# Performance work log

Hardware: AMD Instinct MI355X
Metric: run time of the kernel (lower is better)

Reference implementation:

```python
import jax, jax.numpy as jnp
import numpy as np

N = 100000
DIM = 128
E = 3200000


def setup_inputs() -> dict:
    key = jax.random.key(0)
    k1, k2, k3, k4 = jax.random.split(key, 4)
    x = jax.random.normal(k1, (N, DIM), dtype=jnp.float32)
    edge_index = jax.random.randint(k2, (2, E), 0, N, dtype=jnp.int64)
    # GCNConv params: glorot-style weight [dim, dim], zero-init bias
    W = jax.random.normal(k3, (DIM, DIM), dtype=jnp.float32) * (1.0 / np.sqrt(DIM))
    b = jnp.zeros((DIM,), dtype=jnp.float32)
    return {"x": x, "edge_index": edge_index, "W": W, "b": b}


def gcn_conv(x, edge_index, W, b):
    n = x.shape[0]
    # add self-loops (PyG default add_self_loops=True)
    loop = jnp.arange(n, dtype=edge_index.dtype)
    row = jnp.concatenate([edge_index[0], loop])  # source
    col = jnp.concatenate([edge_index[1], loop])  # target (aggregation index)
    # symmetric normalization D^-1/2 (A+I) D^-1/2; degree counted on targets
    deg = jax.ops.segment_sum(jnp.ones_like(col, dtype=x.dtype), col, num_segments=n)
    dinv = jnp.where(deg > 0, jax.lax.rsqrt(deg), 0.0)
    norm = dinv[row] * dinv[col]  # [E+N]
    xw = x @ W  # dense transform first (dim small)
    msgs = xw[row] * norm[:, None]  # gather + scale
    out = jax.ops.segment_sum(msgs, col, num_segments=n)  # scatter-add
    return out + b


def reference(x, edge_index, W, b):
    # NOTE: original torch loop recomputes from the same x every iteration,
    # so the result equals a single relu(GCNConv(x, edge_index)).
    return jax.nn.relu(gcn_conv(x, edge_index, W, b))
```

## Files before the change

### kernel.cpp

```cpp
#include <hip/hip_runtime.h>

#define DIM 128
#define E_FIXED 3200000
#define BSH 6
#define BNODES 64
#define NB 1600
#define BCAP 2816
#define NBLK 256
#define CAPS 1600
#define XS 136

typedef __attribute__((ext_vector_type(8))) short bf16x8;
typedef __attribute__((ext_vector_type(4))) float f32x4;

__device__ __forceinline__ float bflo(unsigned int w) { return __uint_as_float(w << 16); }
__device__ __forceinline__ float bfhi(unsigned int w) { return __uint_as_float(w & 0xffff0000u); }
__device__ __forceinline__ unsigned short f2bf(float f) {
    union { float f; unsigned int u; } c; c.f = f;
    unsigned int u = c.u + 0x7FFFu + ((c.u >> 16) & 1u);
    return (unsigned short)(u >> 16);
}

__device__ __forceinline__ int edge_shift(const int* __restrict__ edge, int force64) {
    int w = edge[2 * (threadIdx.x & 63) + 1];
    unsigned long long nz = __ballot(w != 0);
    return force64 ? 1 : (nz ? 0 : 1);
}

__global__ __launch_bounds__(1024) void hist_kernel(const int* __restrict__ edge,
                                                    int force64,
                                                    int* __restrict__ hist_g, int E) {
    __shared__ int h[NB];
    const int sh = edge_shift(edge, force64);
    const int tid = threadIdx.x;
    const int k = blockIdx.x;
    for (int b = tid; b < NB; b += 1024) h[b] = 0;
    __syncthreads();

    const int cpb = (E + NBLK - 1) / NBLK;
    const int e0 = k * cpb;
    const int e1 = min(E, e0 + cpb);
    for (int e = e0 + tid; e < e1; e += 1024) {
        int c = edge[((size_t)(E + e)) << sh];
        atomicAdd(&h[c >> BSH], 1);
    }
    __syncthreads();
    for (int b = tid; b < NB; b += 1024) hist_g[(size_t)k * NB + b] = h[b];
}

__global__ __launch_bounds__(NBLK) void prefix_kernel(const int* __restrict__ hist_g,
                                                      int* __restrict__ pre_t,
                                                      int* __restrict__ total) {
    __shared__ int sc[2][NBLK];
    const int b = blockIdx.x;
    const int t = threadIdx.x;
    int v = hist_g[(size_t)t * NB + b];
    sc[0][t] = v;
    __syncthreads();
    int buf = 0;
#pragma unroll
    for (int off = 1; off < NBLK; off <<= 1) {
        sc[buf ^ 1][t] = sc[buf][t] + ((t >= off) ? sc[buf][t - off] : 0);
        buf ^= 1;
        __syncthreads();
    }
    pre_t[(size_t)b * NBLK + t] = sc[buf][t] - v;
    if (t == NBLK - 1) total[b] = sc[buf][t];
}

__global__ __launch_bounds__(512) void scatter_kernel(const int* __restrict__ edge,
                                                      int force64,
                                                      const int* __restrict__ pre_t,
                                                      int* __restrict__ bucketed, int E) {
    __shared__ int cur[NB];
    const int sh = edge_shift(edge, force64);
    const int tid = threadIdx.x;
    const int k = blockIdx.x;
    for (int b = tid; b < NB; b += 512) cur[b] = pre_t[(size_t)b * NBLK + k];
    __syncthreads();

    const int cpb = (E + NBLK - 1) / NBLK;
    const int e0 = k * cpb;
    const int e1 = min(E, e0 + cpb);
    for (int e = e0 + tid; e < e1; e += 512) {
        int r = edge[((size_t)e) << sh];
        int c = edge[((size_t)(E + e)) << sh];
        int b = c >> BSH;
        int pos = atomicAdd(&cur[b], 1);
        if (pos < BCAP)
            bucketed[(size_t)b * BCAP + pos] = (r << BSH) | (c & (BNODES - 1));
    }
}

__global__ __launch_bounds__(256) void degree_kernel(const int* __restrict__ bucketed,
                                                     const int* __restrict__ total,
                                                     int* __restrict__ deg, int n) {
    __shared__ int h[BNODES];
    const int b = blockIdx.x, t = threadIdx.x;
    if (t < BNODES) h[t] = 0;
    __syncthreads();
    const int m = min(total[b], BCAP);
    const int* seg = bucketed + (size_t)b * BCAP;
    for (int i = t; i < m; i += 256) atomicAdd(&h[seg[i] & (BNODES - 1)], 1);
    __syncthreads();
    int gnode = (b << BSH) + t;
    if (t < BNODES && gnode < n) deg[gnode] = h[t];
}

__global__ __launch_bounds__(256) void gemm_kernel(const float* __restrict__ x,
                                                   const float* __restrict__ W,
                                                   const int* __restrict__ deg,
                                                   unsigned short* __restrict__ xws, int n) {
    __shared__ unsigned short xb[64 * XS];
    __shared__ unsigned short wt[128 * XS];
    __shared__ float sdn[64];
    const int tid = threadIdx.x;
    const int base = blockIdx.x * 64;

#pragma unroll
    for (int it = 0; it < 8; ++it) {
        int idx = it * 256 + tid;
        int r = idx >> 5;
        int k4 = idx & 31;
        int gr = base + r;
        float4 v = make_float4(0.f, 0.f, 0.f, 0.f);
        if (gr < n) v = ((const float4*)(x + (size_t)gr * DIM))[k4];
        ushort4 u;
        u.x = f2bf(v.x); u.y = f2bf(v.y); u.z = f2bf(v.z); u.w = f2bf(v.w);
        *(ushort4*)&xb[r * XS + k4 * 4] = u;
    }
#pragma unroll
    for (int it = 0; it < 16; ++it) {
        int idx = it * 256 + tid;
        int k = idx >> 5;
        int c4 = idx & 31;
        float4 v = ((const float4*)(W + (size_t)k * DIM))[c4];
        wt[(c4 * 4 + 0) * XS + k] = f2bf(v.x);
        wt[(c4 * 4 + 1) * XS + k] = f2bf(v.y);
        wt[(c4 * 4 + 2) * XS + k] = f2bf(v.z);
        wt[(c4 * 4 + 3) * XS + k] = f2bf(v.w);
    }
    if (tid < 64) {
        int gn = base + tid;
        int d = (gn < n) ? deg[gn] : 0;
        sdn[tid] = rsqrtf((float)(d + 1));
    }
    __syncthreads();

    const int w = tid >> 6, lane = tid & 63;
    const int lrow = lane & 15, kgrp = lane >> 4;
    const unsigned short* arow = &xb[(w * 16 + lrow) * XS + kgrp * 8];
    const unsigned short* bbase = &wt[lrow * XS + kgrp * 8];

    const int lr0 = w * 16 + kgrp * 4;
    const float dv0 = sdn[lr0 + 0], dv1 = sdn[lr0 + 1];
    const float dv2 = sdn[lr0 + 2], dv3 = sdn[lr0 + 3];
    const int grow0 = base + lr0;

    bf16x8 a0 = *(const bf16x8*)(arow + 0);
    bf16x8 a1 = *(const bf16x8*)(arow + 32);
    bf16x8 a2 = *(const bf16x8*)(arow + 64);
    bf16x8 a3 = *(const bf16x8*)(arow + 96);

#pragma unroll
    for (int ct = 0; ct < 8; ++ct) {
        const unsigned short* bcol = bbase + ct * 16 * XS;
        f32x4 acc = {0.f, 0.f, 0.f, 0.f};
        acc = __builtin_amdgcn_mfma_f32_16x16x32_bf16(a0, *(const bf16x8*)(bcol + 0),  acc, 0, 0, 0);
        acc = __builtin_amdgcn_mfma_f32_16x16x32_bf16(a1, *(const bf16x8*)(bcol + 32), acc, 0, 0, 0);
        acc = __builtin_amdgcn_mfma_f32_16x16x32_bf16(a2, *(const bf16x8*)(bcol + 64), acc, 0, 0, 0);
        acc = __builtin_amdgcn_mfma_f32_16x16x32_bf16(a3, *(const bf16x8*)(bcol + 96), acc, 0, 0, 0);

        int gcol = ct * 16 + lrow;
        if (grow0 + 0 < n) xws[(size_t)(grow0 + 0) * DIM + gcol] = f2bf(acc[0] * dv0);
        if (grow0 + 1 < n) xws[(size_t)(grow0 + 1) * DIM + gcol] = f2bf(acc[1] * dv1);
        if (grow0 + 2 < n) xws[(size_t)(grow0 + 2) * DIM + gcol] = f2bf(acc[2] * dv2);
        if (grow0 + 3 < n) xws[(size_t)(grow0 + 3) * DIM + gcol] = f2bf(acc[3] * dv3);
    }
}

__device__ __forceinline__ void bf8_acc(uint4 u, float4& p, float4& r) {
    p.x += bflo(u.x); p.y += bfhi(u.x);
    p.z += bflo(u.y); p.w += bfhi(u.y);
    r.x += bflo(u.z); r.y += bfhi(u.z);
    r.z += bflo(u.w); r.w += bfhi(u.w);
}

__global__ __launch_bounds__(256) void agg_kernel(const unsigned short* __restrict__ xws,
                                                  const int* __restrict__ bucketed,
                                                  const int* __restrict__ total,
                                                  const int* __restrict__ deg,
                                                  const float* __restrict__ bias,
                                                  float* __restrict__ out, int n) {
    __shared__ int lds_csr[CAPS];
    __shared__ int hcur[32];
    __shared__ int sc[2][32];
    __shared__ int loff[33];
    __shared__ float sdn[32];
    __shared__ float sbias[DIM];

    const int tid = threadIdx.x;
    const int b = blockIdx.x >> 1;
    const int sub = blockIdx.x & 1;
    const int m = min(total[b], BCAP);
    const int* seg = bucketed + (size_t)b * BCAP;
    const int base_node = (b << BSH) + sub * 32;

    if (tid < 32) {
        int gn = base_node + tid;
        int d = (gn < n) ? deg[gn] : 0;
        sc[0][tid] = d;
        hcur[tid] = 0;
        sdn[tid] = rsqrtf((float)(d + 1));
    }
    if (tid < DIM) sbias[tid] = bias[tid];
    __syncthreads();
    int buf = 0;
#pragma unroll
    for (int off = 1; off < 32; off <<= 1) {
        if (tid < 32)
            sc[buf ^ 1][tid] = sc[buf][tid] + ((tid >= off) ? sc[buf][tid - off] : 0);
        buf ^= 1;
        __syncthreads();
    }
    if (tid < 32) loff[tid + 1] = sc[buf][tid];
    if (tid == 0) loff[0] = 0;
    __syncthreads();

    for (int i = tid; i < m; i += 256) {
        int v = seg[i];
        int loc = v & (BNODES - 1);
        if ((loc >> 5) == sub) {
            int pos = atomicAdd(&hcur[loc & 31], 1);
            int idx = loff[loc & 31] + pos;
            if (idx < CAPS) lds_csr[idx] = v >> BSH;
        }
    }
    __syncthreads();

    const int wave = tid >> 6, lane = tid & 63;
    const int q = lane >> 4;
    const int l16 = lane & 15;
    const int d0 = l16 * 8;

    for (int nl = wave * 8; nl < wave * 8 + 8; ++nl) {
        int gnode = base_node + nl;
        if (gnode >= n) break;
        const int s0 = loff[nl], epos = loff[nl + 1];

        float4 a0 = make_float4(0.f, 0.f, 0.f, 0.f), a1 = a0, b0 = a0, b1 = a0;
        if (q == 0) {
            uint4 u = *(const uint4*)&xws[(size_t)gnode * DIM + d0];
            bf8_acc(u, a0, a1);
        }

        const int ng = (epos - s0) >> 4;
        uint4 c0, c1, c2, c3;
        if (ng > 0) {
            int r0 = lds_csr[s0 + q],      r1 = lds_csr[s0 + 4 + q];
            int r2 = lds_csr[s0 + 8 + q],  r3 = lds_csr[s0 + 12 + q];
            c0 = *(const uint4*)&xws[(size_t)r0 * DIM + d0];
            c1 = *(const uint4*)&xws[(size_t)r1 * DIM + d0];
            c2 = *(const uint4*)&xws[(size_t)r2 * DIM + d0];
            c3 = *(const uint4*)&xws[(size_t)r3 * DIM + d0];
        }
        for (int g2 = 1; g2 < ng; ++g2) {
            int eb = s0 + (g2 << 4);
            int r0 = lds_csr[eb + q],      r1 = lds_csr[eb + 4 + q];
            int r2 = lds_csr[eb + 8 + q],  r3 = lds_csr[eb + 12 + q];
            uint4 n0 = *(const uint4*)&xws[(size_t)r0 * DIM + d0];
            uint4 n1 = *(const uint4*)&xws[(size_t)r1 * DIM + d0];
            uint4 n2 = *(const uint4*)&xws[(size_t)r2 * DIM + d0];
            uint4 n3 = *(const uint4*)&xws[(size_t)r3 * DIM + d0];
            bf8_acc(c0, a0, a1); bf8_acc(c1, b0, b1);
            bf8_acc(c2, a0, a1); bf8_acc(c3, b0, b1);
            c0 = n0; c1 = n1; c2 = n2; c3 = n3;
        }
        int e = s0;
        if (ng > 0) {
            bf8_acc(c0, a0, a1); bf8_acc(c1, b0, b1);
            bf8_acc(c2, a0, a1); bf8_acc(c3, b0, b1);
            e = s0 + (ng << 4);
        }
        for (; e + 4 <= epos; e += 4) {
            int r0 = lds_csr[e + q];
            uint4 u0 = *(const uint4*)&xws[(size_t)r0 * DIM + d0];
            bf8_acc(u0, a0, a1);
        }
        for (; e < epos; ++e) {
            if (q == 0) {
                int r = lds_csr[e];
                uint4 u = *(const uint4*)&xws[(size_t)r * DIM + d0];
                bf8_acc(u, a0, a1);
            }
        }

        float t0x = a0.x + b0.x, t0y = a0.y + b0.y, t0z = a0.z + b0.z, t0w = a0.w + b0.w;
        float t1x = a1.x + b1.x, t1y = a1.y + b1.y, t1z = a1.z + b1.z, t1w = a1.w + b1.w;
        t0x += __shfl_xor(t0x, 16); t0y += __shfl_xor(t0y, 16);
        t0z += __shfl_xor(t0z, 16); t0w += __shfl_xor(t0w, 16);
        t1x += __shfl_xor(t1x, 16); t1y += __shfl_xor(t1y, 16);
        t1z += __shfl_xor(t1z, 16); t1w += __shfl_xor(t1w, 16);
        t0x += __shfl_xor(t0x, 32); t0y += __shfl_xor(t0y, 32);
        t0z += __shfl_xor(t0z, 32); t0w += __shfl_xor(t0w, 32);
        t1x += __shfl_xor(t1x, 32); t1y += __shfl_xor(t1y, 32);
        t1z += __shfl_xor(t1z, 32); t1w += __shfl_xor(t1w, 32);

        float dn = sdn[nl];
        if (q == 0) {
            float4 sb = *(const float4*)&sbias[d0];
            float4 o;
            o.x = fmaxf(t0x * dn + sb.x, 0.f);
            o.y = fmaxf(t0y * dn + sb.y, 0.f);
            o.z = fmaxf(t0z * dn + sb.z, 0.f);
            o.w = fmaxf(t0w * dn + sb.w, 0.f);
            *(float4*)&out[(size_t)gnode * DIM + d0] = o;
        } else if (q == 1) {
            float4 sb = *(const float4*)&sbias[d0 + 4];
            float4 o;
            o.x = fmaxf(t1x * dn + sb.x, 0.f);
            o.y = fmaxf(t1y * dn + sb.y, 0.f);
            o.z = fmaxf(t1z * dn + sb.z, 0.f);
            o.w = fmaxf(t1w * dn + sb.w, 0.f);
            *(float4*)&out[(size_t)gnode * DIM + d0 + 4] = o;
        }
    }
}

extern "C" void kernel_launch(void* const* d_in, const int* in_sizes, int n_in,
                              void* d_out, int out_size, void* d_ws, size_t ws_size,
                              hipStream_t stream) {
    const float* x    = (const float*)d_in[0];
    const int*   edge = (const int*)d_in[1];
    const float* W    = (const float*)d_in[2];
    const float* bias = (const float*)d_in[3];
    float* out = (float*)d_out;

    const int n = in_sizes[0] / DIM;
    const int E = (in_sizes[1] == 4 * E_FIXED) ? E_FIXED : in_sizes[1] / 2;
    const int force64 = (in_sizes[1] == 4 * E_FIXED) ? 1 : 0;
    const int nbuck = (n + BNODES - 1) >> BSH;

    char* p = (char*)d_ws;
    auto carve = [&](size_t bytes) { char* r = p; p += (bytes + 255) & ~(size_t)255; return (void*)r; };
    unsigned short* xws = (unsigned short*)carve((size_t)n * DIM * 2);
    int*   deg      = (int*)carve((size_t)n * 4);
    int*   hist_g   = (int*)carve((size_t)NBLK * NB * 4);
    int*   pre_t    = (int*)carve((size_t)NB * NBLK * 4);
    int*   total    = (int*)carve((size_t)NB * 4);
    int*   bucketed = (int*)carve((size_t)NB * BCAP * 4);

    hist_kernel<<<NBLK, 1024, 0, stream>>>(edge, force64, hist_g, E);
    prefix_kernel<<<nbuck, NBLK, 0, stream>>>(hist_g, pre_t, total);
    scatter_kernel<<<NBLK, 512, 0, stream>>>(edge, force64, pre_t, bucketed, E);
    degree_kernel<<<nbuck, 256, 0, stream>>>(bucketed, total, deg, n);
    gemm_kernel<<<(n + 63) / 64, 256, 0, stream>>>(x, W, deg, xws, n);
    agg_kernel<<<nbuck * 2, 256, 0, stream>>>(xws, bucketed, total, deg, bias, out, n);
}
```

Baseline: 215.0 us.

## Fuse histogram, prefix and scatter into one per-block local bucketing kernel

Replaces the global hist/prefix/scatter pipeline with a single kernel in which each edge chunk counts its own buckets in shared memory, computes a local 2048-entry prefix scan, and scatters edges into a per-chunk region with per-block offsets. The degree and aggregation kernels now walk the 256 per-chunk sub-ranges for their bucket, one thread per chunk, instead of a contiguous bucket segment. This removes two kernel launches, the global histogram round trip, and the fixed BCAP capacity limit. In exchange, the consumer reads are serial per thread over short, scattered ranges, which may be less coalesced and unevenly loaded. The scan also adds many barrier steps over 2048 entries.

```diff
diff --git a/kernel.cpp b/kernel.cpp
--- a/kernel.cpp
+++ b/kernel.cpp
@@ -5,7 +5,6 @@
 #define BSH 6
 #define BNODES 64
 #define NB 1600
-#define BCAP 2816
 #define NBLK 256
 #define CAPS 1600
 #define XS 136
@@ -27,81 +26,70 @@
     return force64 ? 1 : (nz ? 0 : 1);
 }
 
-__global__ __launch_bounds__(1024) void hist_kernel(const int* __restrict__ edge,
-                                                    int force64,
-                                                    int* __restrict__ hist_g, int E) {
-    __shared__ int h[NB];
+__global__ __launch_bounds__(512) void scatter_kernel(const int* __restrict__ edge,
+                                                      int force64, int cpb,
+                                                      int* __restrict__ off_g,
+                                                      int* __restrict__ bucketed, int E) {
+    __shared__ int cnt[NB];
+    __shared__ int sc[2][2048];
     const int sh = edge_shift(edge, force64);
     const int tid = threadIdx.x;
     const int k = blockIdx.x;
-    for (int b = tid; b < NB; b += 1024) h[b] = 0;
-    __syncthreads();
-
-    const int cpb = (E + NBLK - 1) / NBLK;
+    for (int b = tid; b < NB; b += 512) cnt[b] = 0;
+    __syncthreads();
+
     const int e0 = k * cpb;
     const int e1 = min(E, e0 + cpb);
-    for (int e = e0 + tid; e < e1; e += 1024) {
+
+    for (int e = e0 + tid; e < e1; e += 512) {
         int c = edge[((size_t)(E + e)) << sh];
-        atomicAdd(&h[c >> BSH], 1);
-    }
-    __syncthreads();
-    for (int b = tid; b < NB; b += 1024) hist_g[(size_t)k * NB + b] = h[b];
-}
-
-__global__ __launch_bounds__(NBLK) void prefix_kernel(const int* __restrict__ hist_g,
-                                                      int* __restrict__ pre_t,
-                                                      int* __restrict__ total) {
-    __shared__ int sc[2][NBLK];
-    const int b = blockIdx.x;
-    const int t = threadIdx.x;
-    int v = hist_g[(size_t)t * NB + b];
-    sc[0][t] = v;
+        atomicAdd(&cnt[c >> BSH], 1);
+    }
+    __syncthreads();
+
+    for (int i = tid; i < 2048; i += 512) sc[0][i] = (i < NB) ? cnt[i] : 0;
     __syncthreads();
     int buf = 0;
-#pragma unroll
-    for (int off = 1; off < NBLK; off <<= 1) {
-        sc[buf ^ 1][t] = sc[buf][t] + ((t >= off) ? sc[buf][t - off] : 0);
+    for (int off = 1; off < 2048; off <<= 1) {
+        for (int i = tid; i < 2048; i += 512)
+            sc[buf ^ 1][i] = sc[buf][i] + ((i >= off) ? sc[buf][i - off] : 0);
         buf ^= 1;
         __syncthreads();
     }
-    pre_t[(size_t)b * NBLK + t] = sc[buf][t] - v;
-    if (t == NBLK - 1) total[b] = sc[buf][t];
-}
-
-__global__ __launch_bounds__(512) void scatter_kernel(const int* __restrict__ edge,
-                                                      int force64,
-                                                      const int* __restrict__ pre_t,
-                                                      int* __restrict__ bucketed, int E) {
-    __shared__ int cur[NB];
-    const int sh = edge_shift(edge, force64);
-    const int tid = threadIdx.x;
-    const int k = blockIdx.x;
-    for (int b = tid; b < NB; b += 512) cur[b] = pre_t[(size_t)b * NBLK + k];
-    __syncthreads();
-
-    const int cpb = (E + NBLK - 1) / NBLK;
-    const int e0 = k * cpb;
-    const int e1 = min(E, e0 + cpb);
+    for (int b = tid; b < NB; b += 512) {
+        int excl = sc[buf][b] - ((b < NB) ? ((b == 0) ? sc[buf][0] : sc[buf][b] - sc[buf][b - 1]) : 0);
+        excl = (b == 0) ? 0 : sc[buf][b - 1];
+        off_g[(size_t)k * (NB + 1) + b] = excl;
+        cnt[b] = excl;
+    }
+    if (tid == 0) off_g[(size_t)k * (NB + 1) + NB] = sc[buf][NB - 1];
+    __syncthreads();
+
+    int* region = bucketed + (size_t)k * cpb;
     for (int e = e0 + tid; e < e1; e += 512) {
         int r = edge[((size_t)e) << sh];
         int c = edge[((size_t)(E + e)) << sh];
         int b = c >> BSH;
-        int pos = atomicAdd(&cur[b], 1);
-        if (pos < BCAP)
-            bucketed[(size_t)b * BCAP + pos] = (r << BSH) | (c & (BNODES - 1));
+        int pos = atomicAdd(&cnt[b], 1);
+        region[pos] = (r << BSH) | (c & (BNODES - 1));
     }
 }
 
 __global__ __launch_bounds__(256) void degree_kernel(const int* __restrict__ bucketed,
-                                                     const int* __restrict__ total,
+                                                     const int* __restrict__ off_g, int cpb,
                                                      int* __restrict__ deg, int n) {
     __shared__ int h[BNODES];
     const int b = blockIdx.x, t = threadIdx.x;
     if (t < BNODES) h[t] = 0;
     __syncthreads();
-    const int m = min(total[b], BCAP);
-    const int* seg = bucketed + (size_t)b * BCAP;
-    for (int i = t; i < m; i += 256) atomicAdd(&h[seg[i] & (BNODES - 1)], 1);
+    {
+        const int k = t;
+        int o0 = off_g[(size_t)k * (NB + 1) + b];
+        int o1 = off_g[(size_t)k * (NB + 1) + b + 1];
+        const int* region = bucketed + (size_t)k * cpb;
+        for (int i = o0; i < o1; ++i)
+            atomicAdd(&h[region[i] & (BNODES - 1)], 1);
+    }
     __syncthreads();
     int gnode = (b << BSH) + t;
     if (t < BNODES && gnode < n) deg[gnode] = h[t];
@@ -188,7 +176,7 @@
 
 __global__ __launch_bounds__(256) void agg_kernel(const unsigned short* __restrict__ xws,
                                                   const int* __restrict__ bucketed,
-                                                  const int* __restrict__ total,
+                                                  const int* __restrict__ off_g, int cpb,
                                                   const int* __restrict__ deg,
                                                   const float* __restrict__ bias,
                                                   float* __restrict__ out, int n) {
@@ -202,8 +190,6 @@
     const int tid = threadIdx.x;
     const int b = blockIdx.x >> 1;
     const int sub = blockIdx.x & 1;
-    const int m = min(total[b], BCAP);
-    const int* seg = bucketed + (size_t)b * BCAP;
     const int base_node = (b << BSH) + sub * 32;
 
     if (tid < 32) {
@@ -227,13 +213,19 @@
     if (tid == 0) loff[0] = 0;
     __syncthreads();
 
-    for (int i = tid; i < m; i += 256) {
-        int v = seg[i];
-        int loc = v & (BNODES - 1);
-        if ((loc >> 5) == sub) {
-            int pos = atomicAdd(&hcur[loc & 31], 1);
-            int idx = loff[loc & 31] + pos;
-            if (idx < CAPS) lds_csr[idx] = v >> BSH;
+    {
+        const int k = tid;
+        int o0 = off_g[(size_t)k * (NB + 1) + b];
+        int o1 = off_g[(size_t)k * (NB + 1) + b + 1];
+        const int* region = bucketed + (size_t)k * cpb;
+        for (int i = o0; i < o1; ++i) {
+            int v = region[i];
+            int loc = v & (BNODES - 1);
+            if ((loc >> 5) == sub) {
+                int pos = atomicAdd(&hcur[loc & 31], 1);
+                int idx = loff[loc & 31] + pos;
+                if (idx < CAPS) lds_csr[idx] = v >> BSH;
+            }
         }
     }
     __syncthreads();
@@ -340,20 +332,17 @@
     const int E = (in_sizes[1] == 4 * E_FIXED) ? E_FIXED : in_sizes[1] / 2;
     const int force64 = (in_sizes[1] == 4 * E_FIXED) ? 1 : 0;
     const int nbuck = (n + BNODES - 1) >> BSH;
+    const int cpb = (E + NBLK - 1) / NBLK;
 
     char* p = (char*)d_ws;
     auto carve = [&](size_t bytes) { char* r = p; p += (bytes + 255) & ~(size_t)255; return (void*)r; };
     unsigned short* xws = (unsigned short*)carve((size_t)n * DIM * 2);
     int*   deg      = (int*)carve((size_t)n * 4);
-    int*   hist_g   = (int*)carve((size_t)NBLK * NB * 4);
-    int*   pre_t    = (int*)carve((size_t)NB * NBLK * 4);
-    int*   total    = (int*)carve((size_t)NB * 4);
-    int*   bucketed = (int*)carve((size_t)NB * BCAP * 4);
-
-    hist_kernel<<<NBLK, 1024, 0, stream>>>(edge, force64, hist_g, E);
-    prefix_kernel<<<nbuck, NBLK, 0, stream>>>(hist_g, pre_t, total);
-    scatter_kernel<<<NBLK, 512, 0, stream>>>(edge, force64, pre_t, bucketed, E);
-    degree_kernel<<<nbuck, 256, 0, stream>>>(bucketed, total, deg, n);
+    int*   off_g    = (int*)carve((size_t)NBLK * (NB + 1) * 4);
+    int*   bucketed = (int*)carve((size_t)NBLK * cpb * 4);
+
+    scatter_kernel<<<NBLK, 512, 0, stream>>>(edge, force64, cpb, off_g, bucketed, E);
+    degree_kernel<<<nbuck, 256, 0, stream>>>(bucketed, off_g, cpb, deg, n);
     gemm_kernel<<<(n + 63) / 64, 256, 0, stream>>>(x, W, deg, xws, n);
-    agg_kernel<<<nbuck * 2, 256, 0, stream>>>(xws, bucketed, total, deg, bias, out, n);
-}
+    agg_kernel<<<nbuck * 2, 256, 0, stream>>>(xws, bucketed, off_g, cpb, deg, bias, out, n);
+}
```

Measured after the change: 280.8 us. 30.6% more time.
